# Performance work log

Hardware: AMD Instinct MI355X
Metric: run time of the kernel (lower is better)

Reference implementation:

```python
import jax, jax.numpy as jnp
import numpy as np

D = 64    # input_dim
N = 64    # num_nodes / num_sensors
S = 256   # scale_num
BS = 16
O = 64    # output_dim
EPS = 1e-5


def _conv1d(x, w, pad):
    # x: [B, Cin, L], w: [Cout, Cin, K]
    return jax.lax.conv_general_dilated(x, w, (1,), [(pad, pad)],
                                        dimension_numbers=('NCH', 'OIH', 'NCH'))


def _bn_ncl(x, g, b):
    # training-mode BatchNorm1d over channel dim of [B, C, L]
    m = x.mean(axis=(0, 2), keepdims=True)
    v = x.var(axis=(0, 2), keepdims=True)  # biased, as torch uses for normalization
    return (x - m) * jax.lax.rsqrt(v + EPS) * g[None, :, None] + b[None, :, None]


def _maxpool2(x):
    return jax.lax.reduce_window(x, -jnp.inf, jax.lax.max,
                                 (1, 1, 2), (1, 1, 2), [(0, 0), (0, 0), (1, 1)])


def _block(x, w, g, b, pad):
    return _maxpool2(jax.nn.relu(_bn_ncl(_conv1d(x, w, pad), g, b)))


def setup_inputs() -> dict:
    key = jax.random.key(0)
    ks = jax.random.split(key, 8)
    def p(k, shape, fan_in):
        return (jax.random.normal(k, shape, jnp.float32) / np.sqrt(fan_in)).astype(jnp.float32)
    return {
        'x': jax.random.normal(ks[0], (BS, S, N, D), jnp.float32),
        'conv1_w': p(ks[1], (4 * D, D, 3), D * 3),
        'bn1_g': jnp.ones(4 * D, jnp.float32), 'bn1_b': jnp.zeros(4 * D, jnp.float32),
        'conv2_w': p(ks[2], (2 * D, 4 * D, 3), 4 * D * 3),
        'bn2_g': jnp.ones(2 * D, jnp.float32), 'bn2_b': jnp.zeros(2 * D, jnp.float32),
        'conv3_w': p(ks[3], (4 * D, 2 * D, 3), 2 * D * 3),
        'bn3_g': jnp.ones(4 * D, jnp.float32), 'bn3_b': jnp.zeros(4 * D, jnp.float32),
        'map_w': p(ks[4], (2 * D, 2 * D), 2 * D), 'map_b': jnp.zeros(2 * D, jnp.float32),
        'theta_w': p(ks[5], (O, 2 * D), 2 * D), 'theta_b': jnp.zeros(O, jnp.float32),
        'bns_g': jnp.ones(O, jnp.float32), 'bns_b': jnp.zeros(O, jnp.float32),
    }


def reference(x, conv1_w, bn1_g, bn1_b, conv2_w, bn2_g, bn2_b,
              conv3_w, bn3_g, bn3_b, map_w, map_b, theta_w, theta_b,
              bns_g, bns_b):
    bs, s, n, d = x.shape
    # ---- Temporal 1D-CNN per node ----
    t = x.transpose(0, 2, 1, 3).reshape(bs * n, s, d).transpose(0, 2, 1)  # [bs*N, D, S]
    t = _block(t, conv1_w, bn1_g, bn1_b, 1)
    t = _block(t, conv2_w, bn2_g, bn2_b, 2)
    t = _block(t, conv3_w, bn3_g, bn3_b, 3)  # [bs*N, 4D, L3]
    l3 = t.shape[-1]
    time_conv = 2 * l3
    tem_out = t.reshape(bs, n, time_conv, 2 * d)
    spa = tem_out.transpose(0, 2, 1, 3).reshape(bs * time_conv, n, 2 * d)
    # ---- Dot-product graph construction ----
    nf = spa @ map_w.T + map_b                       # [B', N, 2D]
    adj = jnp.einsum('bnf,bmf->bnm', nf, nf)         # [B', N, N]
    eye = jnp.eye(n, dtype=x.dtype)
    adj = jax.nn.leaky_relu(adj - eye * 1e8)
    adj = jax.nn.softmax(adj, axis=-1) + eye
    # ---- MPNN (field=1) ----
    out = jnp.einsum('bnm,bmf->bnf', adj, nf) @ theta_w.T + theta_b  # [B', N, O]
    m = out.mean(axis=(0, 1))
    v = out.var(axis=(0, 1))
    out = jax.nn.leaky_relu((out - m) * jax.lax.rsqrt(v + EPS) * bns_g + bns_b)
    # ---- window pooling ----
    g = out.reshape(bs, time_conv // 2, 2, n, O)
    return g.mean(axis=2)  # [bs, num_windows, N, O]
```

## Files before the change

kernel.cpp:

```cpp
#include <hip/hip_runtime.h>


#define TPB 256

#define RAW1 0
#define FIN1 512
#define RAW2 1024
#define FIN2 1280
#define RAW3 1536
#define FIN3 2048
#define RAWG 2560
#define ST_FLOATS 2688

typedef __attribute__((ext_vector_type(8))) short bf16x8;
typedef __attribute__((ext_vector_type(4))) float f32x4;

union U8 { unsigned u[4]; bf16x8 v; };

__device__ __forceinline__ unsigned short bf16tr(float x) {
    return (unsigned short)(__float_as_uint(x) >> 16);
}
__device__ __forceinline__ float bf16tof(unsigned short h) {
    return __uint_as_float(((unsigned int)h) << 16);
}
__device__ __forceinline__ void split2(float a, float b, unsigned& h, unsigned& l) {
    unsigned short ha = bf16tr(a), hb = bf16tr(b);
    unsigned short la = bf16tr(a - bf16tof(ha)), lb = bf16tr(b - bf16tof(hb));
    h = (unsigned)ha | ((unsigned)hb << 16);
    l = (unsigned)la | ((unsigned)lb << 16);
}

__global__ __launch_bounds__(TPB) void split_w_k(const float* __restrict__ w,
                                                 unsigned short* __restrict__ wh,
                                                 unsigned short* __restrict__ wl,
                                                 int CO, int CI)
{
    int idx = blockIdx.x * TPB + threadIdx.x;
    if (idx >= CO * CI * 3) return;
    int ci = idx % CI; int rest = idx / CI; int co = rest % CO; int k = rest / CO;
    float v = w[((size_t)co * CI + ci) * 3 + k];
    unsigned short h = bf16tr(v);
    unsigned short l = bf16tr(v - bf16tof(h));
    wh[idx] = h; wl[idx] = l;
}

__global__ __launch_bounds__(TPB) void split_lin_k(const float* __restrict__ w,
                                                   unsigned short* __restrict__ wh,
                                                   unsigned short* __restrict__ wl,
                                                   int n)
{
    int i = blockIdx.x * TPB + threadIdx.x;
    if (i >= n) return;
    float v = w[i];
    unsigned short h = bf16tr(v);
    wh[i] = h; wl[i] = bf16tr(v - bf16tof(h));
}

template<int LAYOUT, int MODE, int STAGEBN, int CF>
__global__ __launch_bounds__(TPB) void mconv_k(const float* __restrict__ in,
                                               const unsigned short* __restrict__ wh,
                                               const unsigned short* __restrict__ wl,
                                               const float* __restrict__ finIn,
                                               float* __restrict__ out,
                                               float* __restrict__ raw,
                                               int CI, int CO, int Lin, int pad,
                                               int Lconv, int Lp,
                                               int bzStore, int bn0x, int bn0o)
{
    __shared__ __align__(16) unsigned short Xh[66 * 72];
    __shared__ __align__(16) unsigned short Xl[66 * 72];
    __shared__ float s_s1[256], s_s2[256];
    constexpr bool STATS = (MODE == 3 || MODE == 4);

    int tid  = threadIdx.x;
    int lane = tid & 63;
    int w    = tid >> 6;
    int g16  = lane >> 4;
    int l16  = lane & 15;
    int wbase = w * (CF * 16);
    int bz   = blockIdx.z;
    int Lbase = (int)blockIdx.x * 64 - 1;
    int gbase = Lbase - pad;

    const float* base;
    int RS;
    if (LAYOUT == 0) {
        int bn = bn0x + bz;
        base = in + (size_t)(bn >> 6) * 1048576 + (size_t)(bn & 63) * 64;
        RS = 4096;
    } else {
        base = in + (size_t)bz * CI * Lin;
        RS = CI;
    }

    if (STATS && tid < CO) { s_s1[tid] = 0.f; s_s2[tid] = 0.f; }

    f32x4 acc[CF][4];
#pragma unroll
    for (int cf = 0; cf < CF; cf++)
#pragma unroll
        for (int nf = 0; nf < 4; nf++) {
            f32x4 z = {0.f, 0.f, 0.f, 0.f};
            acc[cf][nf] = z;
        }

    for (int ci0 = 0; ci0 < CI; ci0 += 32) {
        __syncthreads();
        for (int idx = tid; idx < 264; idx += TPB) {
            int r = idx >> 2, q = idx & 3;
            int gl = gbase + r;
            float4 va = {0.f, 0.f, 0.f, 0.f}, vb = {0.f, 0.f, 0.f, 0.f};
            if (gl >= 0 && gl < Lin) {
                const float* p = base + (size_t)gl * RS + ci0 + 8 * q;
                va = *(const float4*)p;
                vb = *(const float4*)(p + 4);
                if (STAGEBN) {
                    const float* sc = finIn + ci0 + 8 * q;
                    const float* sh = finIn + CI + ci0 + 8 * q;
                    float4 s0 = *(const float4*)sc, s1 = *(const float4*)(sc + 4);
                    float4 h0 = *(const float4*)sh, h1 = *(const float4*)(sh + 4);
                    va.x = fmaxf(va.x * s0.x + h0.x, 0.f);
                    va.y = fmaxf(va.y * s0.y + h0.y, 0.f);
                    va.z = fmaxf(va.z * s0.z + h0.z, 0.f);
                    va.w = fmaxf(va.w * s0.w + h0.w, 0.f);
                    vb.x = fmaxf(vb.x * s1.x + h1.x, 0.f);
                    vb.y = fmaxf(vb.y * s1.y + h1.y, 0.f);
                    vb.z = fmaxf(vb.z * s1.z + h1.z, 0.f);
                    vb.w = fmaxf(vb.w * s1.w + h1.w, 0.f);
                }
            }
            uint4 hu, lu;
            split2(va.x, va.y, hu.x, lu.x);
            split2(va.z, va.w, hu.y, lu.y);
            split2(vb.x, vb.y, hu.z, lu.z);
            split2(vb.z, vb.w, hu.w, lu.w);
            *(uint4*)&Xh[r * 72 + 8 * q] = hu;
            *(uint4*)&Xl[r * 72 + 8 * q] = lu;
        }
        __syncthreads();

#pragma unroll
        for (int k = 0; k < 3; k++) {
            bf16x8 ah[CF], al[CF];
#pragma unroll
            for (int cf = 0; cf < CF; cf++) {
                size_t wof = ((size_t)(k * CO + wbase + cf * 16 + l16)) * CI
                             + ci0 + g16 * 8;
                ah[cf] = *(const bf16x8*)(wh + wof);
                al[cf] = *(const bf16x8*)(wl + wof);
            }
#pragma unroll
            for (int nf = 0; nf < 4; nf++) {
                if (Lbase + nf * 16 >= Lconv) continue;
                int rb = nf * 16 + l16 + k;
                bf16x8 bh = *(const bf16x8*)&Xh[rb * 72 + g16 * 8];
                bf16x8 bl = *(const bf16x8*)&Xl[rb * 72 + g16 * 8];
#pragma unroll
                for (int cf = 0; cf < CF; cf++) {
                    acc[cf][nf] = __builtin_amdgcn_mfma_f32_16x16x32_bf16(
                        ah[cf], bh, acc[cf][nf], 0, 0, 0);
                    acc[cf][nf] = __builtin_amdgcn_mfma_f32_16x16x32_bf16(
                        ah[cf], bl, acc[cf][nf], 0, 0, 0);
                    acc[cf][nf] = __builtin_amdgcn_mfma_f32_16x16x32_bf16(
                        al[cf], bh, acc[cf][nf], 0, 0, 0);
                }
            }
        }
    }

    if (STATS) {
#pragma unroll
        for (int cf = 0; cf < CF; cf++)
#pragma unroll
            for (int rg = 0; rg < 4; rg++) {
                float a = 0.f, b = 0.f;
#pragma unroll
                for (int nf = 0; nf < 4; nf++) {
                    int l = Lbase + nf * 16 + l16;
                    if (l >= 0 && l < Lconv) {
                        float v = acc[cf][nf][rg];
                        a += v; b += v * v;
                    }
                }
#pragma unroll
                for (int m = 1; m < 16; m <<= 1) {
                    a += __shfl_xor(a, m); b += __shfl_xor(b, m);
                }
                if (l16 == 0) {
                    atomicAdd(&s_s1[wbase + cf * 16 + g16 * 4 + rg], a);
                    atomicAdd(&s_s2[wbase + cf * 16 + g16 * 4 + rg], b);
                }
            }
    }

    if ((MODE == 3 || MODE == 5) && bz < bzStore) {
#pragma unroll
        for (int cf = 0; cf < CF; cf++)
#pragma unroll
            for (int nf = 0; nf < 4; nf++) {
                int l = Lbase + nf * 16 + l16;
                bool ok = (l >= 0 && l < Lconv);
                float4 pv;
#pragma unroll
                for (int rg = 0; rg < 4; rg++) {
                    float v = ok ? acc[cf][nf][rg] : -3.0e38f;
                    float vv = __shfl_xor(v, 1);
                    ((float*)&pv)[rg] = fmaxf(v, vv);
                }
                int j = (l + 1) >> 1;
                if (!(lane & 1) && j < Lp)
                    *(float4*)&out[((size_t)(bn0o + bz) * Lp + j) * CO
                                   + wbase + cf * 16 + g16 * 4] = pv;
            }
    }
    if (MODE == 4) {
#pragma unroll
        for (int cf = 0; cf < CF; cf++)
#pragma unroll
            for (int nf = 0; nf < 4; nf++) {
                int l = Lbase + nf * 16 + l16;
                bool ok = (l >= 0 && l < Lconv);
                int j = (l + 1) >> 1;
#pragma unroll
                for (int rg = 0; rg < 4; rg++) {
                    float v = ok ? acc[cf][nf][rg] : -3.0e38f;
                    float vv = __shfl_xor(v, 1);
                    if (!(lane & 1) && j < Lp) {
                        float pv = fmaxf(v, vv);
                        int co = wbase + cf * 16 + g16 * 4 + rg;
                        int lin = co * 36 + j;
                        int tc = lin >> 7, f = lin & 127;
                        int bq = bz >> 6, n = bz & 63;
                        out[(((size_t)bq * 72 + tc) * 64 + n) * 128 + f] = pv;
                    }
                }
            }
    }

    if (STATS) {
        __syncthreads();
        if (tid < CO) {
            atomicAdd(&raw[tid], s_s1[tid]);
            atomicAdd(&raw[CO + tid], s_s2[tid]);
        }
    }
}

__global__ __launch_bounds__(TPB) void bn_fin_k(const float* __restrict__ raw,
                                                const float* __restrict__ g,
                                                const float* __restrict__ b,
                                                float* __restrict__ fin, int C, float invN)
{
    int c = threadIdx.x + blockIdx.x * TPB;
    if (c < C) {
        float m = raw[c] * invN;
        float v = raw[C + c] * invN - m * m;
        float sc = g[c] * rsqrtf(v + 1e-5f);
        fin[c] = sc;
        fin[C + c] = b[c] - m * sc;
    }
}

#define AJX(n,m) s_adj[(((n) * 64 + (m)) ^ (((n) & 7) << 3))]

__global__ __launch_bounds__(TPB) void graph_f_k(const float* __restrict__ spa,
                                                 const float* __restrict__ fin3,
                                                 const unsigned short* __restrict__ wmh,
                                                 const unsigned short* __restrict__ wml,
                                                 const float* __restrict__ mapb,
                                                 const unsigned short* __restrict__ thh,
                                                 const unsigned short* __restrict__ thl,
                                                 const float* __restrict__ thb,
                                                 float* __restrict__ gout,
                                                 float* __restrict__ rawg)
{
    __shared__ __align__(16) unsigned short NFh[8192], NFl[8192];
    __shared__ __align__(16) float s_adj[4096];
    __shared__ __align__(16) unsigned short Gth[4096], Gtl[4096];
    __shared__ float s_red[256], s_rmax[64], s_rsum[64], s_s1[64], s_s2[64];

    int tid  = threadIdx.x;
    int lane = tid & 63;
    int w    = tid >> 6;
    int g16  = lane >> 4, l16 = lane & 15;
    int n0   = w * 16;
    int bp   = blockIdx.x;
    int tcb  = (bp % 72) * 128;

    if (tid < 64) { s_s1[tid] = 0.f; s_s2[tid] = 0.f; }

    unsigned aH[16], aL[16];
    {
        const float* ar = spa + ((size_t)bp * 64 + n0 + l16) * 128;
#pragma unroll
        for (int kc = 0; kc < 4; kc++) {
            int kb = kc * 32 + g16 * 8;
            float4 x0 = *(const float4*)(ar + kb);
            float4 x1 = *(const float4*)(ar + kb + 4);
            float v[8] = {x0.x, x0.y, x0.z, x0.w, x1.x, x1.y, x1.z, x1.w};
#pragma unroll
            for (int j = 0; j < 8; j++) {
                int co = ((tcb + kb + j) * 29128) >> 20;
                float z = v[j] * fin3[co] + fin3[256 + co];
                v[j] = z > 0.f ? z : 0.f;
            }
            split2(v[0], v[1], aH[kc*4+0], aL[kc*4+0]);
            split2(v[2], v[3], aH[kc*4+1], aL[kc*4+1]);
            split2(v[4], v[5], aH[kc*4+2], aL[kc*4+2]);
            split2(v[6], v[7], aH[kc*4+3], aL[kc*4+3]);
        }
    }

    {
        f32x4 acc[8];
#pragma unroll
        for (int i = 0; i < 8; i++) { f32x4 z = {0.f,0.f,0.f,0.f}; acc[i] = z; }
#pragma unroll
        for (int ff = 0; ff < 8; ff++) {
#pragma unroll
            for (int kc = 0; kc < 4; kc++) {
                U8 ah, al;
#pragma unroll
                for (int u = 0; u < 4; u++) { ah.u[u] = aH[kc*4+u]; al.u[u] = aL[kc*4+u]; }
                size_t wo = (size_t)(ff * 16 + l16) * 128 + kc * 32 + g16 * 8;
                bf16x8 bh = *(const bf16x8*)(wmh + wo);
                bf16x8 bl = *(const bf16x8*)(wml + wo);
                acc[ff] = __builtin_amdgcn_mfma_f32_16x16x32_bf16(ah.v, bh, acc[ff], 0, 0, 0);
                acc[ff] = __builtin_amdgcn_mfma_f32_16x16x32_bf16(ah.v, bl, acc[ff], 0, 0, 0);
                acc[ff] = __builtin_amdgcn_mfma_f32_16x16x32_bf16(al.v, bh, acc[ff], 0, 0, 0);
            }
        }
#pragma unroll
        for (int ff = 0; ff < 8; ff++) {
            float bv = mapb[ff * 16 + l16];
#pragma unroll
            for (int rg = 0; rg < 4; rg++) {
                int n = n0 + g16 * 4 + rg;
                float v = acc[ff][rg] + bv;
                int s = ((n * 128) + ff * 16 + l16) ^ ((n & 7) << 3);
                unsigned short h = bf16tr(v);
                NFh[s] = h;
                NFl[s] = bf16tr(v - bf16tof(h));
            }
        }
    }
    __syncthreads();

    bf16x8 nh[4], nl[4];
#pragma unroll
    for (int kc = 0; kc < 4; kc++) {
        int r = n0 + l16;
        int s = ((r * 128) + kc * 32 + g16 * 8) ^ ((r & 7) << 3);
        nh[kc] = *(const bf16x8*)&NFh[s];
        nl[kc] = *(const bf16x8*)&NFl[s];
    }

    {
        f32x4 aj[4];
#pragma unroll
        for (int i = 0; i < 4; i++) { f32x4 z = {0.f,0.f,0.f,0.f}; aj[i] = z; }
#pragma unroll
        for (int mf = 0; mf < 4; mf++) {
#pragma unroll
            for (int kc = 0; kc < 4; kc++) {
                int r = mf * 16 + l16;
                int s = ((r * 128) + kc * 32 + g16 * 8) ^ ((r & 7) << 3);
                bf16x8 bh = *(const bf16x8*)&NFh[s];
                bf16x8 bl = *(const bf16x8*)&NFl[s];
                aj[mf] = __builtin_amdgcn_mfma_f32_16x16x32_bf16(nh[kc], bh, aj[mf], 0, 0, 0);
                aj[mf] = __builtin_amdgcn_mfma_f32_16x16x32_bf16(nh[kc], bl, aj[mf], 0, 0, 0);
                aj[mf] = __builtin_amdgcn_mfma_f32_16x16x32_bf16(nl[kc], bh, aj[mf], 0, 0, 0);
            }
        }
#pragma unroll
        for (int mf = 0; mf < 4; mf++)
#pragma unroll
            for (int rg = 0; rg < 4; rg++) {
                int n = n0 + g16 * 4 + rg, m = mf * 16 + l16;
                float v = aj[mf][rg];
                if (n == m) v -= 1e8f;
                v = v > 0.f ? v : 0.01f * v;
                AJX(n, m) = v;
            }
    }

    {
        f32x4 gg[4];
#pragma unroll
        for (int i = 0; i < 4; i++) { f32x4 z = {0.f,0.f,0.f,0.f}; gg[i] = z; }
#pragma unroll
        for (int of = 0; of < 4; of++) {
#pragma unroll
            for (int kc = 0; kc < 4; kc++) {
                size_t to = (size_t)(of * 16 + l16) * 128 + kc * 32 + g16 * 8;
                bf16x8 th_ = *(const bf16x8*)(thh + to);
                bf16x8 tl_ = *(const bf16x8*)(thl + to);
                gg[of] = __builtin_amdgcn_mfma_f32_16x16x32_bf16(nh[kc], th_, gg[of], 0, 0, 0);
                gg[of] = __builtin_amdgcn_mfma_f32_16x16x32_bf16(nh[kc], tl_, gg[of], 0, 0, 0);
                gg[of] = __builtin_amdgcn_mfma_f32_16x16x32_bf16(nl[kc], th_, gg[of], 0, 0, 0);
            }
        }
#pragma unroll
        for (int of = 0; of < 4; of++) {
            unsigned short hs[4], ls[4];
#pragma unroll
            for (int rg = 0; rg < 4; rg++) {
                float v = gg[of][rg];
                hs[rg] = bf16tr(v);
                ls[rg] = bf16tr(v - bf16tof(hs[rg]));
            }
            int o = of * 16 + l16;
            int m = n0 + g16 * 4;
            int s = ((o * 64) + m) ^ ((o & 7) << 3);
            uint2 hp, lp;
            hp.x = (unsigned)hs[0] | ((unsigned)hs[1] << 16);
            hp.y = (unsigned)hs[2] | ((unsigned)hs[3] << 16);
            lp.x = (unsigned)ls[0] | ((unsigned)ls[1] << 16);
            lp.y = (unsigned)ls[2] | ((unsigned)ls[3] << 16);
            *(uint2*)&Gth[s] = hp;
            *(uint2*)&Gtl[s] = lp;
        }
    }
    __syncthreads();

    {
        int n = tid >> 2, q = tid & 3;
        float mx = -3.0e38f;
        for (int m = q * 16; m < q * 16 + 16; m++) mx = fmaxf(mx, AJX(n, m));
        s_red[n * 4 + q] = mx;
    }
    __syncthreads();
    if (tid < 64)
        s_rmax[tid] = fmaxf(fmaxf(s_red[tid * 4], s_red[tid * 4 + 1]),
                            fmaxf(s_red[tid * 4 + 2], s_red[tid * 4 + 3]));
    __syncthreads();
    {
        int n = tid >> 2, q = tid & 3;
        float mx = s_rmax[n];
        float sm = 0.f;
        for (int m = q * 16; m < q * 16 + 16; m++) {
            float e = __expf(AJX(n, m) - mx);
            AJX(n, m) = e;
            sm += e;
        }
        s_red[n * 4 + q] = sm;
    }
    __syncthreads();
    if (tid < 64)
        s_rsum[tid] = 1.0f / (s_red[tid * 4] + s_red[tid * 4 + 1] +
                              s_red[tid * 4 + 2] + s_red[tid * 4 + 3]);
    __syncthreads();
    {
        int n = tid >> 2, q = tid & 3;
        float inv = s_rsum[n];
        for (int m = q * 16; m < q * 16 + 16; m++)
            AJX(n, m) = AJX(n, m) * inv + ((n == m) ? 1.f : 0.f);
    }
    __syncthreads();

    {
        f32x4 oacc[4];
#pragma unroll
        for (int i = 0; i < 4; i++) { f32x4 z = {0.f,0.f,0.f,0.f}; oacc[i] = z; }
#pragma unroll
        for (int kc = 0; kc < 2; kc++) {
            int r = n0 + l16;
            int sf = ((r * 64) + kc * 32 + g16 * 8) ^ ((r & 7) << 3);
            float4 p0 = *(const float4*)&s_adj[sf];
            float4 p1 = *(const float4*)&s_adj[sf + 4];
            U8 ah, al;
            split2(p0.x, p0.y, ah.u[0], al.u[0]);
            split2(p0.z, p0.w, ah.u[1], al.u[1]);
            split2(p1.x, p1.y, ah.u[2], al.u[2]);
            split2(p1.z, p1.w, ah.u[3], al.u[3]);
#pragma unroll
            for (int of = 0; of < 4; of++) {
                int o = of * 16 + l16;
                int s = ((o * 64) + kc * 32 + g16 * 8) ^ ((o & 7) << 3);
                bf16x8 gh = *(const bf16x8*)&Gth[s];
                bf16x8 gl = *(const bf16x8*)&Gtl[s];
                oacc[of] = __builtin_amdgcn_mfma_f32_16x16x32_bf16(ah.v, gh, oacc[of], 0, 0, 0);
                oacc[of] = __builtin_amdgcn_mfma_f32_16x16x32_bf16(ah.v, gl, oacc[of], 0, 0, 0);
                oacc[of] = __builtin_amdgcn_mfma_f32_16x16x32_bf16(al.v, gh, oacc[of], 0, 0, 0);
            }
        }
        float* gb = gout + (size_t)bp * 4096;
#pragma unroll
        for (int of = 0; of < 4; of++) {
            float tb = thb[of * 16 + l16];
            float a = 0.f, b = 0.f;
#pragma unroll
            for (int rg = 0; rg < 4; rg++) {
                int n = n0 + g16 * 4 + rg;
                float v = oacc[of][rg] + tb;
                gb[n * 64 + of * 16 + l16] = v;
                a += v; b += v * v;
            }
            a += __shfl_xor(a, 16); a += __shfl_xor(a, 32);
            b += __shfl_xor(b, 16); b += __shfl_xor(b, 32);
            if (g16 == 0) {
                atomicAdd(&s_s1[of * 16 + l16], a);
                atomicAdd(&s_s2[of * 16 + l16], b);
            }
        }
    }
    __syncthreads();
    if (tid < 64) {
        atomicAdd(&rawg[tid], s_s1[tid]);
        atomicAdd(&rawg[64 + tid], s_s2[tid]);
    }
}

__global__ __launch_bounds__(TPB) void final_k(const float* __restrict__ gout,
                                               const float* __restrict__ raw,
                                               const float* __restrict__ g,
                                               const float* __restrict__ b,
                                               float* __restrict__ out)
{
    long idx = (long)blockIdx.x * TPB + threadIdx.x;
    if (idx >= 2359296L) return;
    int o = (int)(idx & 63);
    long t = idx >> 6;
    int n = (int)(t & 63);
    long t2 = t >> 6;
    long wd = t2 % 36;
    long bb = t2 / 36;
    const float invN = 1.0f / 73728.0f;
    float m = raw[o] * invN;
    float var = raw[64 + o] * invN - m * m;
    float scale = g[o] * rsqrtf(var + 1e-5f);
    float shift = b[o] - m * scale;
    long bp = bb * 72 + wd * 2;
    float v0 = gout[(bp * 64 + n) * 64 + o] * scale + shift;
    float v1 = gout[((bp + 1) * 64 + n) * 64 + o] * scale + shift;
    v0 = v0 > 0.f ? v0 : 0.01f * v0;
    v1 = v1 > 0.f ? v1 : 0.01f * v1;
    out[idx] = 0.5f * (v0 + v1);
}

extern "C" void kernel_launch(void* const* d_in, const int* in_sizes, int n_in,
                              void* d_out, int out_size, void* d_ws, size_t ws_size,
                              hipStream_t stream)
{
    (void)in_sizes; (void)n_in; (void)out_size;
    const float* x    = (const float*)d_in[0];
    const float* c1w  = (const float*)d_in[1];
    const float* g1   = (const float*)d_in[2];
    const float* b1   = (const float*)d_in[3];
    const float* c2w  = (const float*)d_in[4];
    const float* g2   = (const float*)d_in[5];
    const float* b2   = (const float*)d_in[6];
    const float* c3w  = (const float*)d_in[7];
    const float* g3   = (const float*)d_in[8];
    const float* b3   = (const float*)d_in[9];
    const float* mapw = (const float*)d_in[10];
    const float* mapb = (const float*)d_in[11];
    const float* thw  = (const float*)d_in[12];
    const float* thb  = (const float*)d_in[13];
    const float* bng  = (const float*)d_in[14];
    const float* bnb  = (const float*)d_in[15];
    float* out = (float*)d_out;
    float* ws  = (float*)d_ws;

    const size_t WSPLIT_USHORT = 540672;
    const size_t MONO_BYTES = ((size_t)33816576 + 8650752 + ST_FLOATS) * 4
                              + WSPLIT_USHORT * 2;
    int nch = (ws_size >= MONO_BYTES) ? 1 : 2;
    size_t P1SZ = (size_t)(nch == 1 ? 1024 : 512) * 33024;

    float* P1   = ws;
    float* P2   = ws + P1SZ;
    float* SPA  = ws;
    float* GOUT = ws + 9437184;
    float* ST   = ws + P1SZ + 8650752;
    unsigned short* WB  = (unsigned short*)(ST + ST_FLOATS);
    unsigned short* WH1 = WB;
    unsigned short* WL1 = WB + 49152;
    unsigned short* WH2 = WB + 98304;
    unsigned short* WL2 = WB + 196608;
    unsigned short* WH3 = WB + 294912;
    unsigned short* WL3 = WB + 393216;
    unsigned short* WMH = WB + 491520;
    unsigned short* WML = WB + 507904;
    unsigned short* THH = WB + 524288;
    unsigned short* THL = WB + 532480;

    hipMemsetAsync((void*)ST, 0, ST_FLOATS * sizeof(float), stream);
    split_w_k<<<192, TPB, 0, stream>>>(c1w, WH1, WL1, 256, 64);
    split_w_k<<<384, TPB, 0, stream>>>(c2w, WH2, WL2, 128, 256);
    split_w_k<<<384, TPB, 0, stream>>>(c3w, WH3, WL3, 256, 128);
    split_lin_k<<<64, TPB, 0, stream>>>(mapw, WMH, WML, 16384);
    split_lin_k<<<32, TPB, 0, stream>>>(thw, THH, THL, 8192);

    if (nch == 1) {
        mconv_k<0, 3, 0, 4><<<dim3(5, 1, 1024), TPB, 0, stream>>>(
            x, WH1, WL1, nullptr, P1, ST + RAW1,
            64, 256, 256, 1, 256, 129, 1024, 0, 0);
        bn_fin_k<<<1, TPB, 0, stream>>>(ST + RAW1, g1, b1, ST + FIN1, 256, 1.0f / 262144.0f);
        mconv_k<1, 3, 1, 2><<<dim3(3, 1, 1024), TPB, 0, stream>>>(
            P1, WH2, WL2, ST + FIN1, P2, ST + RAW2,
            256, 128, 129, 2, 131, 66, 1024, 0, 0);
    } else {
        mconv_k<0, 3, 0, 4><<<dim3(5, 1, 1024), TPB, 0, stream>>>(
            x, WH1, WL1, nullptr, P1, ST + RAW1,
            64, 256, 256, 1, 256, 129, 512, 0, 0);
        bn_fin_k<<<1, TPB, 0, stream>>>(ST + RAW1, g1, b1, ST + FIN1, 256, 1.0f / 262144.0f);
        mconv_k<1, 3, 1, 2><<<dim3(3, 1, 512), TPB, 0, stream>>>(
            P1, WH2, WL2, ST + FIN1, P2, ST + RAW2,
            256, 128, 129, 2, 131, 66, 512, 0, 0);
        mconv_k<0, 5, 0, 4><<<dim3(5, 1, 512), TPB, 0, stream>>>(
            x, WH1, WL1, nullptr, P1, nullptr,
            64, 256, 256, 1, 256, 129, 512, 512, 0);
        mconv_k<1, 3, 1, 2><<<dim3(3, 1, 512), TPB, 0, stream>>>(
            P1, WH2, WL2, ST + FIN1, P2, ST + RAW2,
            256, 128, 129, 2, 131, 66, 512, 0, 512);
    }
    bn_fin_k<<<1, TPB, 0, stream>>>(ST + RAW2, g2, b2, ST + FIN2, 128, 1.0f / 134144.0f);

    mconv_k<1, 4, 1, 4><<<dim3(2, 1, 1024), TPB, 0, stream>>>(
        P2, WH3, WL3, ST + FIN2, SPA, ST + RAW3,
        128, 256, 66, 3, 70, 36, 1024, 0, 0);
    bn_fin_k<<<1, TPB, 0, stream>>>(ST + RAW3, g3, b3, ST + FIN3, 256, 1.0f / 71680.0f);

    graph_f_k<<<1152, TPB, 0, stream>>>(SPA, ST + FIN3, WMH, WML, mapb,
                                        THH, THL, thb, GOUT, ST + RAWG);
    final_k<<<9216, TPB, 0, stream>>>(GOUT, ST + RAWG, bng, bnb, out);
}
```

Measured before the change: 694.3 us.

## Double-buffer conv input tiles and loop over L-tiles inside each block

The conv kernel now stages input tiles in two shared-memory buffers and prefetches the next (L-tile, channel-chunk) slice into registers while MFMAs run on the current one, using a single barrier per step. Each block also walks every L-tile of its sequence instead of launching one block per tile, so the grid shrinks to one block per batch-node. The aim is to hide global load latency and cut the barrier count, at the cost of doubled LDS use, more registers and fewer blocks to fill the GPU.

```diff
diff --git a/kernel.cpp b/kernel.cpp
--- a/kernel.cpp
+++ b/kernel.cpp
@@ -64,11 +64,11 @@
                                                float* __restrict__ out,
                                                float* __restrict__ raw,
                                                int CI, int CO, int Lin, int pad,
-                                               int Lconv, int Lp,
+                                               int Lconv, int Lp, int NT,
                                                int bzStore, int bn0x, int bn0o)
 {
-    __shared__ __align__(16) unsigned short Xh[66 * 72];
-    __shared__ __align__(16) unsigned short Xl[66 * 72];
+    __shared__ __align__(16) unsigned short Xh[2][66 * 72];
+    __shared__ __align__(16) unsigned short Xl[2][66 * 72];
     __shared__ float s_s1[256], s_s2[256];
     constexpr bool STATS = (MODE == 3 || MODE == 4);
 
@@ -79,8 +79,6 @@
     int l16  = lane & 15;
     int wbase = w * (CF * 16);
     int bz   = blockIdx.z;
-    int Lbase = (int)blockIdx.x * 64 - 1;
-    int gbase = Lbase - pad;
 
     const float* base;
     int RS;
@@ -95,50 +93,101 @@
 
     if (STATS && tid < CO) { s_s1[tid] = 0.f; s_s2[tid] = 0.f; }
 
+    const int NC = CI >> 5;
+    const int NS = NT * NC;
+
+    int r0 = tid >> 2, q0 = tid & 3;
+    bool has1 = (tid < 8);
+    int r1 = (tid + 256) >> 2, q1 = tid & 3;
+
+    float v0[8], v1[8];
+
+    auto LOAD = [&](int s) {
+        int t = s / NC, c = s - t * NC;
+        int gb = t * 64 - 1 - pad;
+        {
+            int gl = gb + r0;
+            if (gl >= 0 && gl < Lin) {
+                const float* p = base + (size_t)gl * RS + c * 32 + 8 * q0;
+                float4 a = *(const float4*)p, b4 = *(const float4*)(p + 4);
+                v0[0] = a.x;  v0[1] = a.y;  v0[2] = a.z;  v0[3] = a.w;
+                v0[4] = b4.x; v0[5] = b4.y; v0[6] = b4.z; v0[7] = b4.w;
+            } else {
+#pragma unroll
+                for (int j = 0; j < 8; j++) v0[j] = 0.f;
+            }
+        }
+        if (has1) {
+            int gl = gb + r1;
+            if (gl >= 0 && gl < Lin) {
+                const float* p = base + (size_t)gl * RS + c * 32 + 8 * q1;
+                float4 a = *(const float4*)p, b4 = *(const float4*)(p + 4);
+                v1[0] = a.x;  v1[1] = a.y;  v1[2] = a.z;  v1[3] = a.w;
+                v1[4] = b4.x; v1[5] = b4.y; v1[6] = b4.z; v1[7] = b4.w;
+            } else {
+#pragma unroll
+                for (int j = 0; j < 8; j++) v1[j] = 0.f;
+            }
+        }
+    };
+
+    auto WRITE1 = [&](float* v, int r, int q, int c, int gb, int buf) {
+        if (STAGEBN) {
+            int gl = gb + r;
+            if (gl >= 0 && gl < Lin) {
+                const float* sc = finIn + c * 32 + 8 * q;
+                const float* sh = finIn + CI + c * 32 + 8 * q;
+                float4 s0 = *(const float4*)sc, s1 = *(const float4*)(sc + 4);
+                float4 h0 = *(const float4*)sh, h1 = *(const float4*)(sh + 4);
+                v[0] = fmaxf(v[0] * s0.x + h0.x, 0.f);
+                v[1] = fmaxf(v[1] * s0.y + h0.y, 0.f);
+                v[2] = fmaxf(v[2] * s0.z + h0.z, 0.f);
+                v[3] = fmaxf(v[3] * s0.w + h0.w, 0.f);
+                v[4] = fmaxf(v[4] * s1.x + h1.x, 0.f);
+                v[5] = fmaxf(v[5] * s1.y + h1.y, 0.f);
+                v[6] = fmaxf(v[6] * s1.z + h1.z, 0.f);
+                v[7] = fmaxf(v[7] * s1.w + h1.w, 0.f);
+            }
+        }
+        uint4 hu, lu;
+        split2(v[0], v[1], hu.x, lu.x);
+        split2(v[2], v[3], hu.y, lu.y);
+        split2(v[4], v[5], hu.z, lu.z);
+        split2(v[6], v[7], hu.w, lu.w);
+        *(uint4*)&Xh[buf][r * 72 + 8 * q] = hu;
+        *(uint4*)&Xl[buf][r * 72 + 8 * q] = lu;
+    };
+
+    auto WRITE = [&](int s, int buf) {
+        int t = s / NC, c = s - t * NC;
+        int gb = t * 64 - 1 - pad;
+        WRITE1(v0, r0, q0, c, gb, buf);
+        if (has1) WRITE1(v1, r1, q1, c, gb, buf);
+    };
+
+    LOAD(0);
+    WRITE(0, 0);
+    __syncthreads();
+
     f32x4 acc[CF][4];
-#pragma unroll
-    for (int cf = 0; cf < CF; cf++)
-#pragma unroll
-        for (int nf = 0; nf < 4; nf++) {
-            f32x4 z = {0.f, 0.f, 0.f, 0.f};
-            acc[cf][nf] = z;
-        }
-
-    for (int ci0 = 0; ci0 < CI; ci0 += 32) {
-        __syncthreads();
-        for (int idx = tid; idx < 264; idx += TPB) {
-            int r = idx >> 2, q = idx & 3;
-            int gl = gbase + r;
-            float4 va = {0.f, 0.f, 0.f, 0.f}, vb = {0.f, 0.f, 0.f, 0.f};
-            if (gl >= 0 && gl < Lin) {
-                const float* p = base + (size_t)gl * RS + ci0 + 8 * q;
-                va = *(const float4*)p;
-                vb = *(const float4*)(p + 4);
-                if (STAGEBN) {
-                    const float* sc = finIn + ci0 + 8 * q;
-                    const float* sh = finIn + CI + ci0 + 8 * q;
-                    float4 s0 = *(const float4*)sc, s1 = *(const float4*)(sc + 4);
-                    float4 h0 = *(const float4*)sh, h1 = *(const float4*)(sh + 4);
-                    va.x = fmaxf(va.x * s0.x + h0.x, 0.f);
-                    va.y = fmaxf(va.y * s0.y + h0.y, 0.f);
-                    va.z = fmaxf(va.z * s0.z + h0.z, 0.f);
-                    va.w = fmaxf(va.w * s0.w + h0.w, 0.f);
-                    vb.x = fmaxf(vb.x * s1.x + h1.x, 0.f);
-                    vb.y = fmaxf(vb.y * s1.y + h1.y, 0.f);
-                    vb.z = fmaxf(vb.z * s1.z + h1.z, 0.f);
-                    vb.w = fmaxf(vb.w * s1.w + h1.w, 0.f);
+    int cur = 0;
+
+    for (int s = 0; s < NS; s++) {
+        int t = s / NC, c = s - t * NC;
+        int Lbase = t * 64 - 1;
+        if (c == 0) {
+#pragma unroll
+            for (int cf = 0; cf < CF; cf++)
+#pragma unroll
+                for (int nf = 0; nf < 4; nf++) {
+                    f32x4 z = {0.f, 0.f, 0.f, 0.f};
+                    acc[cf][nf] = z;
                 }
-            }
-            uint4 hu, lu;
-            split2(va.x, va.y, hu.x, lu.x);
-            split2(va.z, va.w, hu.y, lu.y);
-            split2(vb.x, vb.y, hu.z, lu.z);
-            split2(vb.z, vb.w, hu.w, lu.w);
-            *(uint4*)&Xh[r * 72 + 8 * q] = hu;
-            *(uint4*)&Xl[r * 72 + 8 * q] = lu;
-        }
-        __syncthreads();
-
+        }
+
+        if (s + 1 < NS) LOAD(s + 1);
+
+        int ci0 = c * 32;
 #pragma unroll
         for (int k = 0; k < 3; k++) {
             bf16x8 ah[CF], al[CF];
@@ -153,8 +202,8 @@
             for (int nf = 0; nf < 4; nf++) {
                 if (Lbase + nf * 16 >= Lconv) continue;
                 int rb = nf * 16 + l16 + k;
-                bf16x8 bh = *(const bf16x8*)&Xh[rb * 72 + g16 * 8];
-                bf16x8 bl = *(const bf16x8*)&Xl[rb * 72 + g16 * 8];
+                bf16x8 bh = *(const bf16x8*)&Xh[cur][rb * 72 + g16 * 8];
+                bf16x8 bl = *(const bf16x8*)&Xl[cur][rb * 72 + g16 * 8];
 #pragma unroll
                 for (int cf = 0; cf < CF; cf++) {
                     acc[cf][nf] = __builtin_amdgcn_mfma_f32_16x16x32_bf16(
@@ -166,79 +215,83 @@
                 }
             }
         }
+
+        if (c == NC - 1) {
+            if (STATS) {
+#pragma unroll
+                for (int cf = 0; cf < CF; cf++)
+#pragma unroll
+                    for (int rg = 0; rg < 4; rg++) {
+                        float a = 0.f, b = 0.f;
+#pragma unroll
+                        for (int nf = 0; nf < 4; nf++) {
+                            int l = Lbase + nf * 16 + l16;
+                            if (l >= 0 && l < Lconv) {
+                                float v = acc[cf][nf][rg];
+                                a += v; b += v * v;
+                            }
+                        }
+#pragma unroll
+                        for (int m = 1; m < 16; m <<= 1) {
+                            a += __shfl_xor(a, m); b += __shfl_xor(b, m);
+                        }
+                        if (l16 == 0) {
+                            atomicAdd(&s_s1[wbase + cf * 16 + g16 * 4 + rg], a);
+                            atomicAdd(&s_s2[wbase + cf * 16 + g16 * 4 + rg], b);
+                        }
+                    }
+            }
+            if ((MODE == 3 || MODE == 5) && bz < bzStore) {
+#pragma unroll
+                for (int cf = 0; cf < CF; cf++)
+#pragma unroll
+                    for (int nf = 0; nf < 4; nf++) {
+                        int l = Lbase + nf * 16 + l16;
+                        bool ok = (l >= 0 && l < Lconv);
+                        float4 pv;
+#pragma unroll
+                        for (int rg = 0; rg < 4; rg++) {
+                            float v = ok ? acc[cf][nf][rg] : -3.0e38f;
+                            float vv = __shfl_xor(v, 1);
+                            ((float*)&pv)[rg] = fmaxf(v, vv);
+                        }
+                        int j = (l + 1) >> 1;
+                        if (!(lane & 1) && j < Lp)
+                            *(float4*)&out[((size_t)(bn0o + bz) * Lp + j) * CO
+                                           + wbase + cf * 16 + g16 * 4] = pv;
+                    }
+            }
+            if (MODE == 4) {
+#pragma unroll
+                for (int cf = 0; cf < CF; cf++)
+#pragma unroll
+                    for (int nf = 0; nf < 4; nf++) {
+                        int l = Lbase + nf * 16 + l16;
+                        bool ok = (l >= 0 && l < Lconv);
+                        int j = (l + 1) >> 1;
+#pragma unroll
+                        for (int rg = 0; rg < 4; rg++) {
+                            float v = ok ? acc[cf][nf][rg] : -3.0e38f;
+                            float vv = __shfl_xor(v, 1);
+                            if (!(lane & 1) && j < Lp) {
+                                float pv = fmaxf(v, vv);
+                                int co = wbase + cf * 16 + g16 * 4 + rg;
+                                int lin = co * 36 + j;
+                                int tc = lin >> 7, f = lin & 127;
+                                int bq = bz >> 6, n = bz & 63;
+                                out[(((size_t)bq * 72 + tc) * 64 + n) * 128 + f] = pv;
+                            }
+                        }
+                    }
+            }
+        }
+
+        if (s + 1 < NS) WRITE(s + 1, cur ^ 1);
+        __syncthreads();
+        cur ^= 1;
     }
 
     if (STATS) {
-#pragma unroll
-        for (int cf = 0; cf < CF; cf++)
-#pragma unroll
-            for (int rg = 0; rg < 4; rg++) {
-                float a = 0.f, b = 0.f;
-#pragma unroll
-                for (int nf = 0; nf < 4; nf++) {
-                    int l = Lbase + nf * 16 + l16;
-                    if (l >= 0 && l < Lconv) {
-                        float v = acc[cf][nf][rg];
-                        a += v; b += v * v;
-                    }
-                }
-#pragma unroll
-                for (int m = 1; m < 16; m <<= 1) {
-                    a += __shfl_xor(a, m); b += __shfl_xor(b, m);
-                }
-                if (l16 == 0) {
-                    atomicAdd(&s_s1[wbase + cf * 16 + g16 * 4 + rg], a);
-                    atomicAdd(&s_s2[wbase + cf * 16 + g16 * 4 + rg], b);
-                }
-            }
-    }
-
-    if ((MODE == 3 || MODE == 5) && bz < bzStore) {
-#pragma unroll
-        for (int cf = 0; cf < CF; cf++)
-#pragma unroll
-            for (int nf = 0; nf < 4; nf++) {
-                int l = Lbase + nf * 16 + l16;
-                bool ok = (l >= 0 && l < Lconv);
-                float4 pv;
-#pragma unroll
-                for (int rg = 0; rg < 4; rg++) {
-                    float v = ok ? acc[cf][nf][rg] : -3.0e38f;
-                    float vv = __shfl_xor(v, 1);
-                    ((float*)&pv)[rg] = fmaxf(v, vv);
-                }
-                int j = (l + 1) >> 1;
-                if (!(lane & 1) && j < Lp)
-                    *(float4*)&out[((size_t)(bn0o + bz) * Lp + j) * CO
-                                   + wbase + cf * 16 + g16 * 4] = pv;
-            }
-    }
-    if (MODE == 4) {
-#pragma unroll
-        for (int cf = 0; cf < CF; cf++)
-#pragma unroll
-            for (int nf = 0; nf < 4; nf++) {
-                int l = Lbase + nf * 16 + l16;
-                bool ok = (l >= 0 && l < Lconv);
-                int j = (l + 1) >> 1;
-#pragma unroll
-                for (int rg = 0; rg < 4; rg++) {
-                    float v = ok ? acc[cf][nf][rg] : -3.0e38f;
-                    float vv = __shfl_xor(v, 1);
-                    if (!(lane & 1) && j < Lp) {
-                        float pv = fmaxf(v, vv);
-                        int co = wbase + cf * 16 + g16 * 4 + rg;
-                        int lin = co * 36 + j;
-                        int tc = lin >> 7, f = lin & 127;
-                        int bq = bz >> 6, n = bz & 63;
-                        out[(((size_t)bq * 72 + tc) * 64 + n) * 128 + f] = pv;
-                    }
-                }
-            }
-    }
-
-    if (STATS) {
-        __syncthreads();
         if (tid < CO) {
             atomicAdd(&raw[tid], s_s1[tid]);
             atomicAdd(&raw[CO + tid], s_s2[tid]);
@@ -593,33 +646,33 @@
     split_lin_k<<<32, TPB, 0, stream>>>(thw, THH, THL, 8192);
 
     if (nch == 1) {
-        mconv_k<0, 3, 0, 4><<<dim3(5, 1, 1024), TPB, 0, stream>>>(
+        mconv_k<0, 3, 0, 4><<<dim3(1, 1, 1024), TPB, 0, stream>>>(
             x, WH1, WL1, nullptr, P1, ST + RAW1,
-            64, 256, 256, 1, 256, 129, 1024, 0, 0);
+            64, 256, 256, 1, 256, 129, 5, 1024, 0, 0);
         bn_fin_k<<<1, TPB, 0, stream>>>(ST + RAW1, g1, b1, ST + FIN1, 256, 1.0f / 262144.0f);
-        mconv_k<1, 3, 1, 2><<<dim3(3, 1, 1024), TPB, 0, stream>>>(
+        mconv_k<1, 3, 1, 2><<<dim3(1, 1, 1024), TPB, 0, stream>>>(
             P1, WH2, WL2, ST + FIN1, P2, ST + RAW2,
-            256, 128, 129, 2, 131, 66, 1024, 0, 0);
+            256, 128, 129, 2, 131, 66, 3, 1024, 0, 0);
     } else {
-        mconv_k<0, 3, 0, 4><<<dim3(5, 1, 1024), TPB, 0, stream>>>(
+        mconv_k<0, 3, 0, 4><<<dim3(1, 1, 1024), TPB, 0, stream>>>(
             x, WH1, WL1, nullptr, P1, ST + RAW1,
-            64, 256, 256, 1, 256, 129, 512, 0, 0);
+            64, 256, 256, 1, 256, 129, 5, 512, 0, 0);
         bn_fin_k<<<1, TPB, 0, stream>>>(ST + RAW1, g1, b1, ST + FIN1, 256, 1.0f / 262144.0f);
-        mconv_k<1, 3, 1, 2><<<dim3(3, 1, 512), TPB, 0, stream>>>(
+        mconv_k<1, 3, 1, 2><<<dim3(1, 1, 512), TPB, 0, stream>>>(
             P1, WH2, WL2, ST + FIN1, P2, ST + RAW2,
-            256, 128, 129, 2, 131, 66, 512, 0, 0);
-        mconv_k<0, 5, 0, 4><<<dim3(5, 1, 512), TPB, 0, stream>>>(
+            256, 128, 129, 2, 131, 66, 3, 512, 0, 0);
+        mconv_k<0, 5, 0, 4><<<dim3(1, 1, 512), TPB, 0, stream>>>(
             x, WH1, WL1, nullptr, P1, nullptr,
-            64, 256, 256, 1, 256, 129, 512, 512, 0);
-        mconv_k<1, 3, 1, 2><<<dim3(3, 1, 512), TPB, 0, stream>>>(
+            64, 256, 256, 1, 256, 129, 5, 512, 512, 0);
+        mconv_k<1, 3, 1, 2><<<dim3(1, 1, 512), TPB, 0, stream>>>(
             P1, WH2, WL2, ST + FIN1, P2, ST + RAW2,
-            256, 128, 129, 2, 131, 66, 512, 0, 512);
+            256, 128, 129, 2, 131, 66, 3, 512, 0, 512);
     }
     bn_fin_k<<<1, TPB, 0, stream>>>(ST + RAW2, g2, b2, ST + FIN2, 128, 1.0f / 134144.0f);
 
-    mconv_k<1, 4, 1, 4><<<dim3(2, 1, 1024), TPB, 0, stream>>>(
+    mconv_k<1, 4, 1, 4><<<dim3(1, 1, 1024), TPB, 0, stream>>>(
         P2, WH3, WL3, ST + FIN2, SPA, ST + RAW3,
-        128, 256, 66, 3, 70, 36, 1024, 0, 0);
+        128, 256, 66, 3, 70, 36, 2, 1024, 0, 0);
     bn_fin_k<<<1, TPB, 0, stream>>>(ST + RAW3, g3, b3, ST + FIN3, 256, 1.0f / 71680.0f);
 
     graph_f_k<<<1152, TPB, 0, stream>>>(SPA, ST + FIN3, WMH, WML, mapb,
```

Measured after the change: 765.1 us. 10.2% more time.

## Prefetch next input chunk into registers in conv kernel; alias graph LDS buffers

Applied to the files above, without the earlier changes.

The conv kernel's staging loop is now software-pipelined: the global loads for the next 32-channel chunk are issued into registers right after the barrier, so they overlap the MFMA work on the current chunk, and the BN/ReLU and bf16 split are applied when writing to shared memory. Separately, the graph kernel aliases its Gth/Gtl buffers onto NFh/NFl through one shared byte array and adds a barrier, cutting LDS use to allow more resident blocks. The costs are extra registers for the prefetch buffers and a new synchronisation point in the graph kernel.

```diff
diff --git a/kernel.cpp b/kernel.cpp
--- a/kernel.cpp
+++ b/kernel.cpp
@@ -95,6 +95,60 @@
 
     if (STATS && tid < CO) { s_s1[tid] = 0.f; s_s2[tid] = 0.f; }
 
+    const int NC = CI >> 5;
+
+    int r0 = tid >> 2, q0 = tid & 3;
+    bool has1 = (tid < 8);
+    int r1 = (tid + 256) >> 2, q1 = tid & 3;
+    float v0[8], v1[8];
+
+    auto LOAD1 = [&](float* v, int r, int q, int c) {
+        int gl = gbase + r;
+        if (gl >= 0 && gl < Lin) {
+            const float* p = base + (size_t)gl * RS + c * 32 + 8 * q;
+            float4 a = *(const float4*)p, b4 = *(const float4*)(p + 4);
+            v[0] = a.x;  v[1] = a.y;  v[2] = a.z;  v[3] = a.w;
+            v[4] = b4.x; v[5] = b4.y; v[6] = b4.z; v[7] = b4.w;
+        } else {
+#pragma unroll
+            for (int j = 0; j < 8; j++) v[j] = 0.f;
+        }
+    };
+    auto LOAD = [&](int c) {
+        LOAD1(v0, r0, q0, c);
+        if (has1) LOAD1(v1, r1, q1, c);
+    };
+    auto WRITE1 = [&](float* v, int r, int q, int c) {
+        if (STAGEBN) {
+            int gl = gbase + r;
+            if (gl >= 0 && gl < Lin) {
+                const float* sc = finIn + c * 32 + 8 * q;
+                const float* sh = finIn + CI + c * 32 + 8 * q;
+                float4 s0 = *(const float4*)sc, s1 = *(const float4*)(sc + 4);
+                float4 h0 = *(const float4*)sh, h1 = *(const float4*)(sh + 4);
+                v[0] = fmaxf(v[0] * s0.x + h0.x, 0.f);
+                v[1] = fmaxf(v[1] * s0.y + h0.y, 0.f);
+                v[2] = fmaxf(v[2] * s0.z + h0.z, 0.f);
+                v[3] = fmaxf(v[3] * s0.w + h0.w, 0.f);
+                v[4] = fmaxf(v[4] * s1.x + h1.x, 0.f);
+                v[5] = fmaxf(v[5] * s1.y + h1.y, 0.f);
+                v[6] = fmaxf(v[6] * s1.z + h1.z, 0.f);
+                v[7] = fmaxf(v[7] * s1.w + h1.w, 0.f);
+            }
+        }
+        uint4 hu, lu;
+        split2(v[0], v[1], hu.x, lu.x);
+        split2(v[2], v[3], hu.y, lu.y);
+        split2(v[4], v[5], hu.z, lu.z);
+        split2(v[6], v[7], hu.w, lu.w);
+        *(uint4*)&Xh[r * 72 + 8 * q] = hu;
+        *(uint4*)&Xl[r * 72 + 8 * q] = lu;
+    };
+    auto WRITE = [&](int c) {
+        WRITE1(v0, r0, q0, c);
+        if (has1) WRITE1(v1, r1, q1, c);
+    };
+
     f32x4 acc[CF][4];
 #pragma unroll
     for (int cf = 0; cf < CF; cf++)
@@ -104,41 +158,14 @@
             acc[cf][nf] = z;
         }
 
-    for (int ci0 = 0; ci0 < CI; ci0 += 32) {
+    LOAD(0);
+    for (int c = 0; c < NC; c++) {
         __syncthreads();
-        for (int idx = tid; idx < 264; idx += TPB) {
-            int r = idx >> 2, q = idx & 3;
-            int gl = gbase + r;
-            float4 va = {0.f, 0.f, 0.f, 0.f}, vb = {0.f, 0.f, 0.f, 0.f};
-            if (gl >= 0 && gl < Lin) {
-                const float* p = base + (size_t)gl * RS + ci0 + 8 * q;
-                va = *(const float4*)p;
-                vb = *(const float4*)(p + 4);
-                if (STAGEBN) {
-                    const float* sc = finIn + ci0 + 8 * q;
-                    const float* sh = finIn + CI + ci0 + 8 * q;
-                    float4 s0 = *(const float4*)sc, s1 = *(const float4*)(sc + 4);
-                    float4 h0 = *(const float4*)sh, h1 = *(const float4*)(sh + 4);
-                    va.x = fmaxf(va.x * s0.x + h0.x, 0.f);
-                    va.y = fmaxf(va.y * s0.y + h0.y, 0.f);
-                    va.z = fmaxf(va.z * s0.z + h0.z, 0.f);
-                    va.w = fmaxf(va.w * s0.w + h0.w, 0.f);
-                    vb.x = fmaxf(vb.x * s1.x + h1.x, 0.f);
-                    vb.y = fmaxf(vb.y * s1.y + h1.y, 0.f);
-                    vb.z = fmaxf(vb.z * s1.z + h1.z, 0.f);
-                    vb.w = fmaxf(vb.w * s1.w + h1.w, 0.f);
-                }
-            }
-            uint4 hu, lu;
-            split2(va.x, va.y, hu.x, lu.x);
-            split2(va.z, va.w, hu.y, lu.y);
-            split2(vb.x, vb.y, hu.z, lu.z);
-            split2(vb.z, vb.w, hu.w, lu.w);
-            *(uint4*)&Xh[r * 72 + 8 * q] = hu;
-            *(uint4*)&Xl[r * 72 + 8 * q] = lu;
-        }
+        WRITE(c);
         __syncthreads();
-
+        if (c + 1 < NC) LOAD(c + 1);
+
+        int ci0 = c * 32;
 #pragma unroll
         for (int k = 0; k < 3; k++) {
             bf16x8 ah[CF], al[CF];
@@ -274,9 +301,12 @@
                                                  float* __restrict__ gout,
                                                  float* __restrict__ rawg)
 {
-    __shared__ __align__(16) unsigned short NFh[8192], NFl[8192];
-    __shared__ __align__(16) float s_adj[4096];
-    __shared__ __align__(16) unsigned short Gth[4096], Gtl[4096];
+    __shared__ __align__(16) char smem[49152];
+    unsigned short* NFh = (unsigned short*)smem;
+    unsigned short* NFl = (unsigned short*)(smem + 16384);
+    float* s_adj        = (float*)(smem + 32768);
+    unsigned short* Gth = (unsigned short*)smem;
+    unsigned short* Gtl = (unsigned short*)(smem + 16384);
     __shared__ float s_red[256], s_rmax[64], s_rsum[64], s_s1[64], s_s2[64];
 
     int tid  = threadIdx.x;
@@ -383,6 +413,7 @@
                 AJX(n, m) = v;
             }
     }
+    __syncthreads();
 
     {
         f32x4 gg[4];
```

New measurement: 743.4 us. 7.1% more time.
